# Optimization experiments

Hardware: AMD Instinct MI355X
Metric: run time of the kernel (lower is better)

## Reference

```python
import jax, jax.numpy as jnp
import numpy as np

N_HEADS = 16
D_HEAD = 64
N_ROTATE = 32
ROPE_BASE = 10000.0
MAX_LEN = 2048  # round_up_to_multiple_of_256(keep count); static for jit
BATCH, SEQ = 2, 4096


def setup_inputs() -> dict:
    key = jax.random.key(0)
    kq, kk, kv = jax.random.split(key, 3)
    q = jax.random.normal(kq, (BATCH, N_HEADS, MAX_LEN, D_HEAD), jnp.float32)
    k = jax.random.normal(kk, (BATCH, N_HEADS, SEQ, D_HEAD), jnp.float32)
    v = jax.random.normal(kv, (BATCH, N_HEADS, SEQ, D_HEAD), jnp.float32)
    # causal full mask [batch, seq, seq] and full position ids [batch, seq]
    mask_full = jnp.broadcast_to(jnp.tril(jnp.ones((SEQ, SEQ), bool)), (BATCH, SEQ, SEQ))
    pos_full = jnp.broadcast_to(jnp.arange(SEQ, dtype=jnp.int32), (BATCH, SEQ))
    # skip_mask: exactly MAX_LEN kept tokens per row (random positions)
    rng = np.random.default_rng(0)
    sm = np.zeros((BATCH, SEQ), dtype=bool)
    for i in range(BATCH):
        sm[i, rng.permutation(SEQ)[:MAX_LEN]] = True
    return {"q": q, "k": k, "v": v, "mask_full": mask_full,
            "pos_full": pos_full, "skip_mask": jnp.asarray(sm)}


def _rope_rotate(x, pos):
    # x: [b, h, L, n_rotate], pos: [b, L]
    half = N_ROTATE // 2
    inv_freq = 1.0 / (ROPE_BASE ** (jnp.arange(0, N_ROTATE, 2, dtype=jnp.float32) / N_ROTATE))
    freqs = pos.astype(jnp.float32)[..., None] * inv_freq          # [b, L, half]
    emb = jnp.concatenate([freqs, freqs], axis=-1)[:, None]        # [b, 1, L, n_rotate]
    cos, sin = jnp.cos(emb), jnp.sin(emb)
    x1, x2 = x[..., :half], x[..., half:]
    rot = jnp.concatenate([-x2, x1], axis=-1)                      # rotate_half
    return x * cos + rot * sin


def reference(q, k, v, mask_full, pos_full, skip_mask):
    b, S = skip_mask.shape
    lengths = skip_mask.sum(axis=1)
    # vectorized _trim_attention_mask: stable argsort compacts kept indices to the front
    order = jnp.argsort(jnp.where(skip_mask, 0, 1), axis=1, stable=True)
    idx = order[:, :MAX_LEN]                                       # [b, max_len]
    brow = jnp.arange(b)[:, None]
    mask_trim = mask_full[brow, idx]                               # [b, max_len, S]
    pos_trim = pos_full[brow, idx]                                 # [b, max_len]
    valid = jnp.arange(MAX_LEN)[None, :] < lengths[:, None]
    mask_trim = mask_trim & valid[..., None]
    pos_trim = jnp.where(valid, pos_trim, 0)

    # partial RoPE on first n_rotate channels
    rq = _rope_rotate(q[..., :N_ROTATE], pos_trim)
    rk = _rope_rotate(k[..., :N_ROTATE], pos_full)
    q = jnp.concatenate([rq, q[..., N_ROTATE:]], axis=-1)
    k = jnp.concatenate([rk, k[..., N_ROTATE:]], axis=-1)

    # masked SDPA (bool mask broadcast over heads)
    scale = 1.0 / jnp.sqrt(jnp.float32(D_HEAD))
    scores = jnp.einsum('bhqd,bhkd->bhqk', q, k) * scale
    scores = jnp.where(mask_trim[:, None], scores, jnp.finfo(scores.dtype).min)
    attn = jax.nn.softmax(scores, axis=-1)
    return jnp.einsum('bhqk,bhkd->bhqd', attn, v)
```

## Files before the change

### kernel.cpp

```cpp
#include <hip/hip_runtime.h>
#include <math.h>

#define BB 2
#define HH 16
#define QQ 2048
#define SS 4096
#define DD 64
#define NRH 16
#define NQT 32

typedef unsigned short u16;
typedef unsigned int   u32;
typedef short bhalf8 __attribute__((ext_vector_type(8)));
typedef float f32x4  __attribute__((ext_vector_type(4)));

typedef __attribute__((address_space(1))) const u32 gu32;
typedef __attribute__((address_space(3))) u32 lu32;

#if __has_builtin(__builtin_amdgcn_exp2f)
#define EXP2(x) __builtin_amdgcn_exp2f(x)
#else
#define EXP2(x) exp2f(x)
#endif

union Frag16 { uint4 u; bhalf8 v; u16 s[8]; uint2 d[2]; };

__device__ __forceinline__ u16 f2bf(float f) {
  union { float f; u32 u; } c; c.f = f;
  return (u16)((c.u + 0x7FFFu + ((c.u >> 16) & 1u)) >> 16);
}

__device__ __forceinline__ u32 cvt_pk_bf16(float lo, float hi) {
  u32 r;
  asm("v_cvt_pk_bf16_f32 %0, %1, %2" : "=v"(r) : "v"(lo), "v"(hi));
  return r;
}

__device__ __forceinline__ bhalf8 ldfrag(const u16* p) {
  Frag16 f; f.u = *reinterpret_cast<const uint4*>(p); return f.v;
}

__device__ __forceinline__ void rope32(float* x, int pos) {
  const float step = 0.8304820237218405f;
  const float fp = (float)pos;
#pragma unroll
  for (int i = 0; i < NRH; ++i) {
    float ang = fp * exp2f(-step * (float)i);
    float sv, cv;
    __sincosf(ang, &sv, &cv);
    float a = x[i], b = x[i + NRH];
    x[i]       = a * cv - b * sv;
    x[i + NRH] = b * cv + a * sv;
  }
}

__device__ __forceinline__ void prep_idx_body(const unsigned char* __restrict__ sm,
                                              int* __restrict__ idx, int b,
                                              int* wsum, int* modes) {
  const int tid = threadIdx.x;

  int c = 0;
  for (int i = 0; i < 32; ++i) c += (sm[tid * 32 + i] != 0) ? 1 : 0;
#pragma unroll
  for (int off = 32; off; off >>= 1) c += __shfl_down(c, off);
  if ((tid & 63) == 0) wsum[tid >> 6] = c;
  __syncthreads();
  if (tid == 0) *modes = (wsum[0] + wsum[1] + wsum[2] + wsum[3] > 3000) ? 1 : 0;
  __syncthreads();
  const bool byteMode = (*modes != 0);
  const u32* sm32 = (const u32*)sm;

  const int base = b * SS + tid * 16;
  u32 flags = 0;
  for (int i = 0; i < 16; ++i) {
    bool f = byteMode ? (sm[base + i] != 0) : (sm32[base + i] != 0);
    flags |= ((u32)(f ? 1 : 0)) << i;
  }
  int cnt = __popc(flags);
  int vv = cnt;
#pragma unroll
  for (int off = 1; off < 64; off <<= 1) {
    int t = __shfl_up(vv, off);
    if ((tid & 63) >= off) vv += t;
  }
  __syncthreads();
  if ((tid & 63) == 63) wsum[tid >> 6] = vv;
  __syncthreads();
  int add = 0;
  for (int w2 = 0; w2 < (tid >> 6); ++w2) add += wsum[w2];
  int p = vv - cnt + add;
  for (int i = 0; i < 16; ++i) {
    if (flags & (1u << i)) {
      if (p < QQ) idx[b * QQ + p] = tid * 16 + i;
      ++p;
    }
  }
}

__global__ void prep_idx_kernel(const unsigned char* __restrict__ sm,
                                int* __restrict__ idx) {
  __shared__ int wsum[4];
  __shared__ int modes;
  prep_idx_body(sm, idx, (int)blockIdx.x, wsum, &modes);
}

__global__ __launch_bounds__(256) void prep_fused_kernel(
    const float* __restrict__ k, const float* __restrict__ v,
    const unsigned char* __restrict__ skip,
    u16* __restrict__ kbf, u16* __restrict__ vfrag, int* __restrict__ idx) {
  __shared__ u16 tile[64][72];
  __shared__ int wsum[4];
  __shared__ int modes;
  if (blockIdx.x >= 2560) {
    prep_idx_body(skip, idx, (int)blockIdx.x - 2560, wsum, &modes);
  } else if (blockIdx.x < 512) {
    int r = blockIdx.x * 256 + threadIdx.x;
    int pos = r & (SS - 1);
    float x[64];
    const float4* src = (const float4*)(k + (size_t)r * DD);
#pragma unroll
    for (int i = 0; i < 16; ++i) {
      float4 t = src[i];
      x[4 * i] = t.x; x[4 * i + 1] = t.y; x[4 * i + 2] = t.z; x[4 * i + 3] = t.w;
    }
    rope32(x, pos);
    u16 tmp[64];
#pragma unroll
    for (int i = 0; i < 64; ++i) tmp[i] = f2bf(x[i]);
    uint4* dst = (uint4*)(kbf + (size_t)r * DD);
#pragma unroll
    for (int i = 0; i < 8; ++i) dst[i] = ((uint4*)tmp)[i];
  } else {
    int blk = (int)blockIdx.x - 512;
    int bh = blk >> 6;
    int jt = blk & 63;
    int t = threadIdx.x;
    int jl = t >> 2;
    int dc = (t & 3) * 16;
    const float4* src = (const float4*)(v + ((size_t)(bh * SS + jt * 64 + jl)) * DD + dc);
#pragma unroll
    for (int i = 0; i < 4; ++i) {
      float4 f = src[i];
      tile[jl][dc + 4 * i]     = f2bf(f.x);
      tile[jl][dc + 4 * i + 1] = f2bf(f.y);
      tile[jl][dc + 4 * i + 2] = f2bf(f.z);
      tile[jl][dc + 4 * i + 3] = f2bf(f.w);
    }
    __syncthreads();
    int d = t >> 2;
    int c4 = t & 3;
    u16 o[16];
#pragma unroll
    for (int m = 0; m < 16; ++m) {
      int p = c4 * 16 + m;
      int kp = (p & 32) | ((p & 4) << 2) | ((p >> 1) & 12) | (p & 3);
      o[m] = tile[kp][d];
    }
    char* tb = (char*)vfrag + (size_t)bh * (SS * DD * 2) + (size_t)jt * 8192;
    {
      int ch = 2 * c4;
      int j = ((d >> 4) << 1) + (ch >> 2);
      char* dst = tb + j * 1024 + (((ch & 3) * 16 + (d & 15)) * 16);
      *(uint4*)dst = ((uint4*)o)[0];
    }
    {
      int ch = 2 * c4 + 1;
      int j = ((d >> 4) << 1) + (ch >> 2);
      char* dst = tb + j * 1024 + (((ch & 3) * 16 + (d & 15)) * 16);
      *(uint4*)dst = ((uint4*)o)[1];
    }
  }
}

__device__ __forceinline__ void stage_k(const char* kb_bh, u16* Kb, int t0,
                                        int w, int srow, int schk) {
#pragma unroll
  for (int p2 = 0; p2 < 2; ++p2) {
    const int rr = w * 16 + p2 * 8 + srow;
    const char* g = kb_bh + (size_t)(t0 + rr) * 128 + ((schk ^ (rr & 7)) * 16);
    lu32* l = (lu32*)((char*)Kb + (w * 16 + p2 * 8) * 128);
    __builtin_amdgcn_global_load_lds((gu32*)g, l, 16, 0, 0);
  }
}

template <bool MASKED>
__device__ __forceinline__ void attn_tile(
    const u16* __restrict__ Kb, const char* __restrict__ vf_lane,
    int t0, int grp, int col, int bnd,
    bhalf8 qa0, bhalf8 qa1,
    f32x4& acc0, f32x4& acc1, f32x4& acc2, f32x4& acc3,
    float& lsum) {
  const int swz = col & 7;

  const char* vf = vf_lane + (size_t)(t0 >> 6) * 8192;
  bhalf8 x0 = ldfrag((const u16*)(vf + 0 * 1024));
  bhalf8 y0 = ldfrag((const u16*)(vf + 1 * 1024));
  bhalf8 x1 = ldfrag((const u16*)(vf + 2 * 1024));
  bhalf8 y1 = ldfrag((const u16*)(vf + 3 * 1024));
  bhalf8 x2 = ldfrag((const u16*)(vf + 4 * 1024));
  bhalf8 y2 = ldfrag((const u16*)(vf + 5 * 1024));
  bhalf8 x3 = ldfrag((const u16*)(vf + 6 * 1024));
  bhalf8 y3 = ldfrag((const u16*)(vf + 7 * 1024));

  f32x4 z = {0.f, 0.f, 0.f, 0.f};
  f32x4 s0 = z, s1 = z, s2 = z, s3 = z;
  {
    const u16* kr0 = Kb + (0 * 16 + col) * 64;
    const u16* kr1 = Kb + (1 * 16 + col) * 64;
    const u16* kr2 = Kb + (2 * 16 + col) * 64;
    const u16* kr3 = Kb + (3 * 16 + col) * 64;
    __builtin_amdgcn_s_setprio(1);
    bhalf8 a0 = ldfrag(kr0 + ((grp ^ swz) * 8));
    s0 = __builtin_amdgcn_mfma_f32_16x16x32_bf16(a0, qa0, s0, 0, 0, 0);
    bhalf8 b0 = ldfrag(kr0 + (((4 + grp) ^ swz) * 8));
    s0 = __builtin_amdgcn_mfma_f32_16x16x32_bf16(b0, qa1, s0, 0, 0, 0);
    bhalf8 a1 = ldfrag(kr1 + ((grp ^ swz) * 8));
    s1 = __builtin_amdgcn_mfma_f32_16x16x32_bf16(a1, qa0, s1, 0, 0, 0);
    bhalf8 b1 = ldfrag(kr1 + (((4 + grp) ^ swz) * 8));
    s1 = __builtin_amdgcn_mfma_f32_16x16x32_bf16(b1, qa1, s1, 0, 0, 0);
    bhalf8 a2 = ldfrag(kr2 + ((grp ^ swz) * 8));
    s2 = __builtin_amdgcn_mfma_f32_16x16x32_bf16(a2, qa0, s2, 0, 0, 0);
    bhalf8 b2 = ldfrag(kr2 + (((4 + grp) ^ swz) * 8));
    s2 = __builtin_amdgcn_mfma_f32_16x16x32_bf16(b2, qa1, s2, 0, 0, 0);
    bhalf8 a3 = ldfrag(kr3 + ((grp ^ swz) * 8));
    s3 = __builtin_amdgcn_mfma_f32_16x16x32_bf16(a3, qa0, s3, 0, 0, 0);
    bhalf8 b3 = ldfrag(kr3 + (((4 + grp) ^ swz) * 8));
    s3 = __builtin_amdgcn_mfma_f32_16x16x32_bf16(b3, qa1, s3, 0, 0, 0);
    __builtin_amdgcn_s_setprio(0);
  }

  uint2 w0, w1, w2, w3;
#define SM_C(SC, CB, W)                                                        \
  {                                                                            \
    float p0, p1, p2v, p3;                                                     \
    const int kb = t0 + (CB) + grp * 4;                                        \
    if (MASKED) {                                                              \
      p0  = (kb + 0 <= bnd) ? EXP2(SC[0] - 16.f) : 0.f;                        \
      p1  = (kb + 1 <= bnd) ? EXP2(SC[1] - 16.f) : 0.f;                        \
      p2v = (kb + 2 <= bnd) ? EXP2(SC[2] - 16.f) : 0.f;                        \
      p3  = (kb + 3 <= bnd) ? EXP2(SC[3] - 16.f) : 0.f;                        \
    } else {                                                                   \
      p0  = EXP2(SC[0] - 16.f);                                                \
      p1  = EXP2(SC[1] - 16.f);                                                \
      p2v = EXP2(SC[2] - 16.f);                                                \
      p3  = EXP2(SC[3] - 16.f);                                                \
    }                                                                          \
    lsum += (p0 + p1) + (p2v + p3);                                            \
    W.x = cvt_pk_bf16(p0, p1);                                                 \
    W.y = cvt_pk_bf16(p2v, p3);                                                \
  }
  SM_C(s0, 0,  w0)
  SM_C(s1, 16, w1)
  SM_C(s2, 32, w2)
  SM_C(s3, 48, w3)
#undef SM_C

  bhalf8 pv0, pv1;
  {
    Frag16 f0, f1;
    f0.d[0] = w0; f0.d[1] = w1;
    f1.d[0] = w2; f1.d[1] = w3;
    pv0 = f0.v; pv1 = f1.v;
  }

  {
    __builtin_amdgcn_s_setprio(1);
    acc0 = __builtin_amdgcn_mfma_f32_16x16x32_bf16(x0, pv0, acc0, 0, 0, 0);
    acc0 = __builtin_amdgcn_mfma_f32_16x16x32_bf16(y0, pv1, acc0, 0, 0, 0);
    acc1 = __builtin_amdgcn_mfma_f32_16x16x32_bf16(x1, pv0, acc1, 0, 0, 0);
    acc1 = __builtin_amdgcn_mfma_f32_16x16x32_bf16(y1, pv1, acc1, 0, 0, 0);
    acc2 = __builtin_amdgcn_mfma_f32_16x16x32_bf16(x2, pv0, acc2, 0, 0, 0);
    acc2 = __builtin_amdgcn_mfma_f32_16x16x32_bf16(y2, pv1, acc2, 0, 0, 0);
    acc3 = __builtin_amdgcn_mfma_f32_16x16x32_bf16(x3, pv0, acc3, 0, 0, 0);
    acc3 = __builtin_amdgcn_mfma_f32_16x16x32_bf16(y3, pv1, acc3, 0, 0, 0);
    __builtin_amdgcn_s_setprio(0);
  }
}

__global__ __launch_bounds__(256, 4) void attn_mfma_kernel(
    const float* __restrict__ qsrc, const u16* __restrict__ kbf,
    const u16* __restrict__ vfrag, const int* __restrict__ idx,
    float* __restrict__ out) {
  __shared__ u16 KbufA[64 * 64];
  __shared__ u16 KbufB[64 * 64];

  const int blk = (int)blockIdx.x;
  const int bh  = blk & 31;
  const int rank = blk >> 5;
  const int rmod = rank & 7;
  const int rdiv = rank >> 3;
  const int qt = (rdiv == 0) ? (31 - rmod)
               : (rdiv == 1) ? rmod
               : (rdiv == 2) ? (23 - rmod)
               : (8 + rmod);
  const int q0  = qt * 64;
  const int b   = bh >> 4;
  const int tid  = threadIdx.x;
  const int w    = tid >> 6;
  const int lane = tid & 63;
  const int grp  = lane >> 4;
  const int col  = lane & 15;

  const char* kb_bh = (const char*)(kbf + (size_t)bh * SS * DD);
  const char* vf_lane = (const char*)vfrag + (size_t)bh * (SS * DD * 2) + (size_t)lane * 16;

  const int srow = lane >> 3;
  const int schk = lane & 7;

  const int* idxb = idx + b * QQ + q0;
  const int bnd = idxb[w * 16 + col];
  const int wave_minb = idxb[w * 16];
  const int wave_maxb = idxb[w * 16 + 15];
  const int maxbound  = idxb[63];
  const int ntiles = (maxbound >> 6) + 1;

  bhalf8 qa0, qa1;
  {
    const int qrow = q0 + w * 16 + col;
    const float* qr = qsrc + (size_t)(bh * QQ + qrow) * DD;
    const int lof = (grp & 1) * 8;
    float4 A0 = *(const float4*)(qr + lof);
    float4 A1 = *(const float4*)(qr + lof + 4);
    float4 B0 = *(const float4*)(qr + 16 + lof);
    float4 B1 = *(const float4*)(qr + 16 + lof + 4);
    float4 C0 = *(const float4*)(qr + 32 + grp * 8);
    float4 C1 = *(const float4*)(qr + 32 + grp * 8 + 4);
    float xlo[8] = {A0.x, A0.y, A0.z, A0.w, A1.x, A1.y, A1.z, A1.w};
    float xhi[8] = {B0.x, B0.y, B0.z, B0.w, B1.x, B1.y, B1.z, B1.w};
    float xq1[8] = {C0.x, C0.y, C0.z, C0.w, C1.x, C1.y, C1.z, C1.w};
    const float scq = 0.125f * 1.44269504088896f;
    const float fp = (float)bnd;
    Frag16 f0, f1;
#pragma unroll
    for (int j = 0; j < 8; ++j) {
      float ang = fp * exp2f(-0.8304820237218405f * (float)(lof + j));
      float sv, cv;
      __sincosf(ang, &sv, &cv);
      float val = (grp >= 2) ? (xhi[j] * cv + xlo[j] * sv)
                             : (xlo[j] * cv - xhi[j] * sv);
      f0.s[j] = f2bf(val * scq);
      f1.s[j] = f2bf(xq1[j] * scq);
    }
    qa0 = f0.v; qa1 = f1.v;
  }

  f32x4 z = {0.f, 0.f, 0.f, 0.f};
  f32x4 acc0 = z, acc1 = z, acc2 = z, acc3 = z;
  float lsum = 0.f;

#define ATTN_CALL(M, KB, T0)                                                   \
  attn_tile<M>(KB, vf_lane, T0, grp, col, bnd, qa0, qa1, acc0, acc1, acc2, acc3, lsum)

  stage_k(kb_bh, KbufA, 0, w, srow, schk);
  __syncthreads();

  for (int ti = 0; ti < ntiles; ti += 2) {
    const bool has1 = (ti + 1) < ntiles;
    if (has1) stage_k(kb_bh, KbufB, (ti + 1) << 6, w, srow, schk);
    {
      const int t0 = ti << 6;
      if (t0 <= wave_maxb) {
        if (t0 + 63 <= wave_minb) ATTN_CALL(false, KbufA, t0);
        else                      ATTN_CALL(true,  KbufA, t0);
      }
    }
    __syncthreads();
    if (has1) {
      if (ti + 2 < ntiles)
        stage_k(kb_bh, KbufA, (ti + 2) << 6, w, srow, schk);
      {
        const int t0 = (ti + 1) << 6;
        if (t0 <= wave_maxb) {
          if (t0 + 63 <= wave_minb) ATTN_CALL(false, KbufB, t0);
          else                      ATTN_CALL(true,  KbufB, t0);
        }
      }
      __syncthreads();
    }
  }
#undef ATTN_CALL

  lsum += __shfl_xor(lsum, 16);
  lsum += __shfl_xor(lsum, 32);
  const float inv = 1.f / lsum;
  float* ob = out + (size_t)(bh * QQ + q0 + w * 16 + col) * DD + grp * 4;
  {
    float4 t;
    t.x = acc0[0] * inv; t.y = acc0[1] * inv; t.z = acc0[2] * inv; t.w = acc0[3] * inv;
    *(float4*)(ob + 0) = t;
    t.x = acc1[0] * inv; t.y = acc1[1] * inv; t.z = acc1[2] * inv; t.w = acc1[3] * inv;
    *(float4*)(ob + 16) = t;
    t.x = acc2[0] * inv; t.y = acc2[1] * inv; t.z = acc2[2] * inv; t.w = acc2[3] * inv;
    *(float4*)(ob + 32) = t;
    t.x = acc3[0] * inv; t.y = acc3[1] * inv; t.z = acc3[2] * inv; t.w = acc3[3] * inv;
    *(float4*)(ob + 48) = t;
  }
}

__global__ __launch_bounds__(64) void attn_fb_kernel(const float* __restrict__ q,
                                                     const float* __restrict__ ksrc,
                                                     const float* __restrict__ v,
                                                     const int* __restrict__ idx,
                                                     float* __restrict__ out) {
  int t = (int)(gridDim.x - 1u - blockIdx.x);
  int sub = t >> 5;
  int bh = t & 31;
  int b = bh >> 4;
  int lane = threadIdx.x;
  int qi = sub * 64 + lane;
  const int bound = idx[b * QQ + qi];

  float qreg[64];
  {
    const float4* qp = (const float4*)(q + ((size_t)bh * QQ + qi) * DD);
#pragma unroll
    for (int i = 0; i < 16; ++i) {
      float4 t4 = qp[i];
      qreg[4 * i] = t4.x; qreg[4 * i + 1] = t4.y;
      qreg[4 * i + 2] = t4.z; qreg[4 * i + 3] = t4.w;
    }
  }
  rope32(qreg, bound);
#pragma unroll
  for (int i = 0; i < 64; ++i) qreg[i] *= 0.125f;

  const float* kbase = ksrc + (size_t)bh * SS * DD;
  const float* vbase = v + (size_t)bh * SS * DD;
  float acc[64];
#pragma unroll
  for (int i = 0; i < 64; ++i) acc[i] = 0.f;
  float mrun = -INFINITY, lrun = 0.f;

  for (int j = 0; j <= bound; ++j) {
    float ka[64];
    const float4* kp = (const float4*)(kbase + (size_t)j * DD);
#pragma unroll
    for (int i = 0; i < 16; ++i) {
      float4 t4 = kp[i];
      ka[4 * i] = t4.x; ka[4 * i + 1] = t4.y;
      ka[4 * i + 2] = t4.z; ka[4 * i + 3] = t4.w;
    }
    rope32(ka, j);
    float s0 = 0.f, s1 = 0.f, s2 = 0.f, s3 = 0.f;
#pragma unroll
    for (int i = 0; i < 16; ++i) {
      s0 = fmaf(qreg[4 * i], ka[4 * i], s0);
      s1 = fmaf(qreg[4 * i + 1], ka[4 * i + 1], s1);
      s2 = fmaf(qreg[4 * i + 2], ka[4 * i + 2], s2);
      s3 = fmaf(qreg[4 * i + 3], ka[4 * i + 3], s3);
    }
    float sc = (s0 + s1) + (s2 + s3);
    if (sc > mrun) {
      float alpha = __expf(mrun - sc);
      lrun *= alpha;
#pragma unroll
      for (int i = 0; i < 64; ++i) acc[i] *= alpha;
      mrun = sc;
    }
    float pw = __expf(sc - mrun);
    lrun += pw;
    const float4* vp = (const float4*)(vbase + (size_t)j * DD);
#pragma unroll
    for (int i = 0; i < 16; ++i) {
      float4 t4 = vp[i];
      acc[4 * i] = fmaf(pw, t4.x, acc[4 * i]);
      acc[4 * i + 1] = fmaf(pw, t4.y, acc[4 * i + 1]);
      acc[4 * i + 2] = fmaf(pw, t4.z, acc[4 * i + 2]);
      acc[4 * i + 3] = fmaf(pw, t4.w, acc[4 * i + 3]);
    }
  }
  float inv = 1.0f / lrun;
  float4* op = (float4*)(out + ((size_t)bh * QQ + qi) * DD);
#pragma unroll
  for (int i = 0; i < 16; ++i) {
    float4 t4;
    t4.x = acc[4 * i] * inv; t4.y = acc[4 * i + 1] * inv;
    t4.z = acc[4 * i + 2] * inv; t4.w = acc[4 * i + 3] * inv;
    op[i] = t4;
  }
}

extern "C" void kernel_launch(void* const* d_in, const int* in_sizes, int n_in,
                              void* d_out, int out_size, void* d_ws, size_t ws_size,
                              hipStream_t stream) {
  (void)in_sizes; (void)n_in; (void)out_size;
  const float* q = (const float*)d_in[0];
  const float* k = (const float*)d_in[1];
  const float* v = (const float*)d_in[2];
  const unsigned char* skip = (const unsigned char*)d_in[5];
  float* out = (float*)d_out;

  char* base = (char*)d_ws;
  int* idx = (int*)base;
  const size_t kbytes = (size_t)BB * HH * SS * DD * 2;
  u16* kbf = (u16*)(base + 16384);
  u16* vfb = (u16*)(base + 16384 + kbytes);
  const size_t need = 16384 + 2 * kbytes;

  if (ws_size >= need) {
    prep_fused_kernel<<<512 + BB * HH * 64 + BB, 256, 0, stream>>>(k, v, skip,
                                                                   kbf, vfb, idx);
    attn_mfma_kernel<<<NQT * 32, 256, 0, stream>>>(q, kbf, vfb, idx, out);
  } else {
    prep_idx_kernel<<<2, 256, 0, stream>>>(skip, idx);
    attn_fb_kernel<<<1024, 64, 0, stream>>>(q, k, v, idx, out);
  }
}
```

Baseline: 287.5 us.

## Software-pipeline PV matmul one tile behind QK and coalesce V fragment writes

The PV MFMA for each tile is deferred and issued after the next tile's QK MFMAs, so softmax exp work can overlap with matrix-core work across tiles. Previous P fragments and V fragments are carried in registers between steps, with a final flush after the loop. The V pre-transpose kernel is also rewritten so each wave writes contiguous 16-byte chunks per lane, making the global stores coalesced. The cost is higher register pressure from the carried fragments, which may reduce occupancy under the 4-blocks launch bound.

```diff
diff --git a/kernel.cpp b/kernel.cpp
--- a/kernel.cpp
+++ b/kernel.cpp
@@ -147,27 +147,22 @@
       tile[jl][dc + 4 * i + 3] = f2bf(f.w);
     }
     __syncthreads();
-    int d = t >> 2;
-    int c4 = t & 3;
-    u16 o[16];
-#pragma unroll
-    for (int m = 0; m < 16; ++m) {
-      int p = c4 * 16 + m;
-      int kp = (p & 32) | ((p & 4) << 2) | ((p >> 1) & 12) | (p & 3);
-      o[m] = tile[kp][d];
-    }
+    const int lane = t & 63;
+    const int jj = t >> 6;
     char* tb = (char*)vfrag + (size_t)bh * (SS * DD * 2) + (size_t)jt * 8192;
-    {
-      int ch = 2 * c4;
-      int j = ((d >> 4) << 1) + (ch >> 2);
-      char* dst = tb + j * 1024 + (((ch & 3) * 16 + (d & 15)) * 16);
-      *(uint4*)dst = ((uint4*)o)[0];
-    }
-    {
-      int ch = 2 * c4 + 1;
-      int j = ((d >> 4) << 1) + (ch >> 2);
-      char* dst = tb + j * 1024 + (((ch & 3) * 16 + (d & 15)) * 16);
-      *(uint4*)dst = ((uint4*)o)[1];
+#pragma unroll
+    for (int h = 0; h < 2; ++h) {
+      int j = jj + h * 4;
+      int d = ((j >> 1) << 4) + (lane & 15);
+      int ch = ((j & 1) << 2) + (lane >> 4);
+      u16 o[8];
+#pragma unroll
+      for (int i = 0; i < 8; ++i) {
+        int p = ch * 8 + i;
+        int kp = (p & 32) | ((p & 4) << 2) | ((p >> 1) & 12) | (p & 3);
+        o[i] = tile[kp][d];
+      }
+      *(uint4*)(tb + j * 1024 + lane * 16) = *((uint4*)o);
     }
   }
 }
@@ -183,24 +178,44 @@
   }
 }
 
+__device__ __forceinline__ void pv_flush(
+    bhalf8 px0, bhalf8 py0, bhalf8 px1, bhalf8 py1,
+    bhalf8 px2, bhalf8 py2, bhalf8 px3, bhalf8 py3,
+    bhalf8 ppv0, bhalf8 ppv1,
+    f32x4& acc0, f32x4& acc1, f32x4& acc2, f32x4& acc3) {
+  __builtin_amdgcn_s_setprio(1);
+  acc0 = __builtin_amdgcn_mfma_f32_16x16x32_bf16(px0, ppv0, acc0, 0, 0, 0);
+  acc0 = __builtin_amdgcn_mfma_f32_16x16x32_bf16(py0, ppv1, acc0, 0, 0, 0);
+  acc1 = __builtin_amdgcn_mfma_f32_16x16x32_bf16(px1, ppv0, acc1, 0, 0, 0);
+  acc1 = __builtin_amdgcn_mfma_f32_16x16x32_bf16(py1, ppv1, acc1, 0, 0, 0);
+  acc2 = __builtin_amdgcn_mfma_f32_16x16x32_bf16(px2, ppv0, acc2, 0, 0, 0);
+  acc2 = __builtin_amdgcn_mfma_f32_16x16x32_bf16(py2, ppv1, acc2, 0, 0, 0);
+  acc3 = __builtin_amdgcn_mfma_f32_16x16x32_bf16(px3, ppv0, acc3, 0, 0, 0);
+  acc3 = __builtin_amdgcn_mfma_f32_16x16x32_bf16(py3, ppv1, acc3, 0, 0, 0);
+  __builtin_amdgcn_s_setprio(0);
+}
+
 template <bool MASKED>
-__device__ __forceinline__ void attn_tile(
+__device__ __forceinline__ void tile_step(
     const u16* __restrict__ Kb, const char* __restrict__ vf_lane,
     int t0, int grp, int col, int bnd,
-    bhalf8 qa0, bhalf8 qa1,
+    bhalf8 qa0, bhalf8 qa1, bool flushPrev,
+    bhalf8& px0, bhalf8& py0, bhalf8& px1, bhalf8& py1,
+    bhalf8& px2, bhalf8& py2, bhalf8& px3, bhalf8& py3,
+    bhalf8& ppv0, bhalf8& ppv1,
     f32x4& acc0, f32x4& acc1, f32x4& acc2, f32x4& acc3,
     float& lsum) {
   const int swz = col & 7;
 
   const char* vf = vf_lane + (size_t)(t0 >> 6) * 8192;
-  bhalf8 x0 = ldfrag((const u16*)(vf + 0 * 1024));
-  bhalf8 y0 = ldfrag((const u16*)(vf + 1 * 1024));
-  bhalf8 x1 = ldfrag((const u16*)(vf + 2 * 1024));
-  bhalf8 y1 = ldfrag((const u16*)(vf + 3 * 1024));
-  bhalf8 x2 = ldfrag((const u16*)(vf + 4 * 1024));
-  bhalf8 y2 = ldfrag((const u16*)(vf + 5 * 1024));
-  bhalf8 x3 = ldfrag((const u16*)(vf + 6 * 1024));
-  bhalf8 y3 = ldfrag((const u16*)(vf + 7 * 1024));
+  bhalf8 nx0 = ldfrag((const u16*)(vf + 0 * 1024));
+  bhalf8 ny0 = ldfrag((const u16*)(vf + 1 * 1024));
+  bhalf8 nx1 = ldfrag((const u16*)(vf + 2 * 1024));
+  bhalf8 ny1 = ldfrag((const u16*)(vf + 3 * 1024));
+  bhalf8 nx2 = ldfrag((const u16*)(vf + 4 * 1024));
+  bhalf8 ny2 = ldfrag((const u16*)(vf + 5 * 1024));
+  bhalf8 nx3 = ldfrag((const u16*)(vf + 6 * 1024));
+  bhalf8 ny3 = ldfrag((const u16*)(vf + 7 * 1024));
 
   f32x4 z = {0.f, 0.f, 0.f, 0.f};
   f32x4 s0 = z, s1 = z, s2 = z, s3 = z;
@@ -229,6 +244,10 @@
     __builtin_amdgcn_s_setprio(0);
   }
 
+  if (flushPrev)
+    pv_flush(px0, py0, px1, py1, px2, py2, px3, py3, ppv0, ppv1,
+             acc0, acc1, acc2, acc3);
+
   uint2 w0, w1, w2, w3;
 #define SM_C(SC, CB, W)                                                        \
   {                                                                            \
@@ -255,26 +274,14 @@
   SM_C(s3, 48, w3)
 #undef SM_C
 
-  bhalf8 pv0, pv1;
   {
     Frag16 f0, f1;
     f0.d[0] = w0; f0.d[1] = w1;
     f1.d[0] = w2; f1.d[1] = w3;
-    pv0 = f0.v; pv1 = f1.v;
-  }
-
-  {
-    __builtin_amdgcn_s_setprio(1);
-    acc0 = __builtin_amdgcn_mfma_f32_16x16x32_bf16(x0, pv0, acc0, 0, 0, 0);
-    acc0 = __builtin_amdgcn_mfma_f32_16x16x32_bf16(y0, pv1, acc0, 0, 0, 0);
-    acc1 = __builtin_amdgcn_mfma_f32_16x16x32_bf16(x1, pv0, acc1, 0, 0, 0);
-    acc1 = __builtin_amdgcn_mfma_f32_16x16x32_bf16(y1, pv1, acc1, 0, 0, 0);
-    acc2 = __builtin_amdgcn_mfma_f32_16x16x32_bf16(x2, pv0, acc2, 0, 0, 0);
-    acc2 = __builtin_amdgcn_mfma_f32_16x16x32_bf16(y2, pv1, acc2, 0, 0, 0);
-    acc3 = __builtin_amdgcn_mfma_f32_16x16x32_bf16(x3, pv0, acc3, 0, 0, 0);
-    acc3 = __builtin_amdgcn_mfma_f32_16x16x32_bf16(y3, pv1, acc3, 0, 0, 0);
-    __builtin_amdgcn_s_setprio(0);
-  }
+    ppv0 = f0.v; ppv1 = f1.v;
+  }
+  px0 = nx0; py0 = ny0; px1 = nx1; py1 = ny1;
+  px2 = nx2; py2 = ny2; px3 = nx3; py3 = ny3;
 }
 
 __global__ __launch_bounds__(256, 4) void attn_mfma_kernel(
@@ -348,8 +355,16 @@
   f32x4 acc0 = z, acc1 = z, acc2 = z, acc3 = z;
   float lsum = 0.f;
 
-#define ATTN_CALL(M, KB, T0)                                                   \
-  attn_tile<M>(KB, vf_lane, T0, grp, col, bnd, qa0, qa1, acc0, acc1, acc2, acc3, lsum)
+  bhalf8 zz = {0, 0, 0, 0, 0, 0, 0, 0};
+  bhalf8 px0 = zz, py0 = zz, px1 = zz, py1 = zz;
+  bhalf8 px2 = zz, py2 = zz, px3 = zz, py3 = zz;
+  bhalf8 ppv0 = zz, ppv1 = zz;
+  bool pend = false;
+
+#define TILE_STEP(M, KB, T0)                                                   \
+  tile_step<M>(KB, vf_lane, T0, grp, col, bnd, qa0, qa1, pend,                 \
+               px0, py0, px1, py1, px2, py2, px3, py3, ppv0, ppv1,             \
+               acc0, acc1, acc2, acc3, lsum)
 
   stage_k(kb_bh, KbufA, 0, w, srow, schk);
   __syncthreads();
@@ -360,8 +375,9 @@
     {
       const int t0 = ti << 6;
       if (t0 <= wave_maxb) {
-        if (t0 + 63 <= wave_minb) ATTN_CALL(false, KbufA, t0);
-        else                      ATTN_CALL(true,  KbufA, t0);
+        if (t0 + 63 <= wave_minb) TILE_STEP(false, KbufA, t0);
+        else                      TILE_STEP(true,  KbufA, t0);
+        pend = true;
       }
     }
     __syncthreads();
@@ -371,14 +387,19 @@
       {
         const int t0 = (ti + 1) << 6;
         if (t0 <= wave_maxb) {
-          if (t0 + 63 <= wave_minb) ATTN_CALL(false, KbufB, t0);
-          else                      ATTN_CALL(true,  KbufB, t0);
+          if (t0 + 63 <= wave_minb) TILE_STEP(false, KbufB, t0);
+          else                      TILE_STEP(true,  KbufB, t0);
+          pend = true;
         }
       }
       __syncthreads();
     }
   }
-#undef ATTN_CALL
+#undef TILE_STEP
+
+  if (pend)
+    pv_flush(px0, py0, px1, py1, px2, py2, px3, py3, ppv0, ppv1,
+             acc0, acc1, acc2, acc3);
 
   lsum += __shfl_xor(lsum, 16);
   lsum += __shfl_xor(lsum, 32);
```

After: 321.1 us. 1.12x slower.
